# Kernel tuning notes

Measured on AMD Instinct MI355X. Metric: run time of the kernel, lower is better.

## Reference

```python
import jax, jax.numpy as jnp
from jax import lax
import numpy as np


def _lstm_stack(sequence, Wx, Wh, b):
    """Standard single-layer LSTM; returns all hidden states [B, T, H]."""
    B, T, I = sequence.shape
    H = Wh.shape[0]
    # Precompute input projection for all timesteps: [B, T, 4H]
    x_proj = jnp.einsum('bti,ih->bth', sequence, Wx) + b

    def step(carry, xt):  # xt: [B, 4H]
        h, c = carry
        z = xt + h @ Wh
        i, f, g, o = jnp.split(z, 4, axis=-1)
        i = jax.nn.sigmoid(i)
        f = jax.nn.sigmoid(f)
        g = jnp.tanh(g)
        o = jax.nn.sigmoid(o)
        c = f * c + i * g
        h = o * jnp.tanh(c)
        return (h, c), h

    h0 = jnp.zeros((B, H), dtype=sequence.dtype)
    c0 = jnp.zeros((B, H), dtype=sequence.dtype)
    (_, _), ys = lax.scan(step, (h0, c0), jnp.transpose(x_proj, (1, 0, 2)))
    return jnp.transpose(ys, (1, 0, 2))  # [B, T, H]


def setup_inputs() -> dict:
    key = jax.random.key(0)
    ks = jax.random.split(key, 6)
    B, T, I, H, K = 64, 256, 512, 1024, 512
    sequence = jax.random.normal(ks[0], (B, T, I), dtype=jnp.float32)
    n_iter = jax.random.randint(ks[1], (B,), 0, T, dtype=jnp.int32)
    Wx = jax.random.normal(ks[2], (I, 4 * H), dtype=jnp.float32) * 0.05
    Wh = jax.random.normal(ks[3], (H, 4 * H), dtype=jnp.float32) * 0.05
    b = jnp.zeros((4 * H,), dtype=jnp.float32)
    codebook = jax.random.normal(ks[4], (K, H), dtype=jnp.float32)
    return {"sequence": sequence, "n_iter": n_iter, "Wx": Wx, "Wh": Wh,
            "b": b, "codebook": codebook}


def reference(sequence, n_iter, Wx, Wh, b, codebook):
    B = sequence.shape[0]
    lstm_stack = _lstm_stack(sequence, Wx, Wh, b)          # [B, T, H]
    unquantized = lstm_stack[jnp.arange(B), n_iter]         # [B, H] batched gather
    # VQ: L2 distance to each codebook vector, argmin, embed lookup
    diff = unquantized[:, None, :] - codebook[None, :, :]   # [B, K, H]
    distance = jnp.linalg.norm(diff, axis=-1)               # [B, K]
    nearest_codebook_idxs = jnp.argmin(distance, axis=-1)   # [B]
    quantized = codebook[nearest_codebook_idxs]             # [B, H]
    return nearest_codebook_idxs, quantized, unquantized
```

## Files before the change

kernel.cpp:

```cpp
#include <hip/hip_runtime.h>
#include <hip/hip_cooperative_groups.h>

namespace cg = cooperative_groups;

typedef unsigned short u16;
typedef unsigned int   u32;
typedef unsigned long long u64;
typedef __attribute__((ext_vector_type(8))) short short8;
typedef __attribute__((ext_vector_type(4))) float f32x4;

#define BB   64
#define TT   256
#define II   512
#define HH   1024
#define KCB  512
#define GH   4096
#define KTOT 1536

#define BPAD 1544

#define WS_WT   0
#define WS_H    (GH*KTOT)
#define WS_DIST (WS_H + 131072)
#define WS_BARC (WS_DIST + BB*KCB)
#define WS_BART (WS_BARC + 8*9*32)

#define LD_AG(p)   __hip_atomic_load((p), __ATOMIC_RELAXED, __HIP_MEMORY_SCOPE_AGENT)
#define ST_AG(p,v) __hip_atomic_store((p), (v), __ATOMIC_RELAXED, __HIP_MEMORY_SCOPE_AGENT)

__device__ __forceinline__ float sigf(float x){ return 1.0f/(1.0f+expf(-x)); }
__device__ __forceinline__ u16 bf16r(float f){ u32 u = __float_as_uint(f); u += 0x7FFFu + ((u>>16)&1u); return (u16)(u>>16); }
__device__ __forceinline__ float bf16f(u16 h){ return __uint_as_float(((u32)h)<<16); }

__device__ __forceinline__ void bar_arrive(u32* bar, int bid, int tid, int e){
    asm volatile("s_waitcnt vmcnt(0)" ::: "memory");
    __syncthreads();
    if (tid == 0) {
        u32 old = atomicAdd(bar + (bid & 7) * 32, 1u);
        if (old == (u32)(e * 32 - 1)) {
            u32 old2 = atomicAdd(bar + 8 * 32, 1u);
            if (old2 == (u32)(e * 8 - 1)) {
                #pragma unroll
                for (int gg = 0; gg < 8; ++gg)
                    ST_AG(bar + (9 + gg) * 32, (u32)e);
            }
        }
    }
}
__device__ __forceinline__ void bar_wait(u32* bar, int bid, int tid, int e){
    if (tid == 0) {
        while ((int)LD_AG(bar + (9 + (bid & 7)) * 32) < e)
            __builtin_amdgcn_s_sleep(1);
        __builtin_amdgcn_fence(__ATOMIC_ACQUIRE, "agent");
    }
    __syncthreads();
}

__global__ __launch_bounds__(512, 1)
void lstm_vq(const float* __restrict__ seq, const int* __restrict__ nit,
             const float* __restrict__ Wx, const float* __restrict__ Wh,
             const float* __restrict__ bias, const float* __restrict__ cb,
             float* __restrict__ out, float* __restrict__ ws)
{
    cg::grid_group grid = cg::this_grid();
    __shared__ __align__(16) u16 bHi[16*BPAD];
    __shared__ __align__(16) u16 bLo[16*BPAD];
    __shared__ __align__(16) float exs[8*1024];
    __shared__ int permL[64], snitL[64];
    __shared__ int sBest;

    const int tid = threadIdx.x;
    const int l   = tid & 63;
    const int w   = tid >> 6;
    const int bid = (int)blockIdx.x;

    float* WT   = ws + WS_WT;
    u16*   hbuf = (u16*)(ws + WS_H);
    float* dist = ws + WS_DIST;
    u32*   barC = (u32*)(ws + WS_BARC);
    u32*   barT = (u32*)(ws + WS_BART);
    float* qz   = out + BB;
    float* uq   = out + BB + BB*HH;

    if (bid == 0) {
        for (int i = tid; i < 8*9*32 + 17*32; i += 512) ST_AG(barC + i, 0u);
    }

    {
        const int c0 = bid * 16;
        float* tile = (float*)bHi;
        for (int kt = 0; kt < KTOT; kt += 64) {
            __syncthreads();
            #pragma unroll
            for (int ii2 = 0; ii2 < 2; ++ii2) {
                int ky = ii2*32 + (tid>>4);
                int cx = tid & 15;
                int kk = kt + ky;
                float v = (kk < II) ? Wx[(size_t)kk*GH + c0 + cx]
                                    : Wh[(size_t)(kk-II)*GH + c0 + cx];
                tile[cx*68 + ky] = v;
            }
            __syncthreads();
            {
                int cx = tid >> 5;
                int k2 = (tid & 31) * 2;
                WT[(size_t)(c0+cx)*KTOT + kt + k2]     = tile[cx*68 + k2];
                WT[(size_t)(c0+cx)*KTOT + kt + k2 + 1] = tile[cx*68 + k2 + 1];
            }
        }
        grid.sync();
    }

    {
        __syncthreads();
        const int n  = tid >> 5;
        const int zc = ((n>>2)<<10) + (bid<<2) + (n&3);
        const float* wr = WT + (size_t)zc*KTOT;
        for (int k = (tid&31)*8; k < KTOT; k += 256) {
            f32x4 v0 = *(const f32x4*)(wr + k);
            f32x4 v1 = *(const f32x4*)(wr + k + 4);
            short8 ph, pl;
            #pragma unroll
            for (int e = 0; e < 8; ++e) {
                float fv = (e<4) ? v0[e] : v1[e-4];
                u16 hb = bf16r(fv);
                ph[e] = (short)hb;
                pl[e] = (short)bf16r(fv - bf16f(hb));
            }
            *(short8*)&bHi[n*BPAD + k] = ph;
            *(short8*)&bLo[n*BPAD + k] = pl;
        }
    }

    {
        if (w == 0) {
            int ni = nit[l];
            int r  = 0;
            #pragma unroll
            for (int j = 0; j < 64; ++j) {
                int nj = __shfl(ni, j, 64);
                r += (nj > ni || (nj == ni && j < l)) ? 1 : 0;
            }
            permL[r] = l;
            snitL[r] = ni;
        }
        __syncthreads();
    }

    const int rEx  = (tid & 255) >> 2;
    const int ccEx = tid & 3;
    const int hcol = (bid<<2) + ccEx;
    const int prG  = permL[rEx];
    const int myNs = snitL[rEx];

    const int tmx0 = __builtin_amdgcn_readfirstlane(snitL[0]);
    const int tmx1 = __builtin_amdgcn_readfirstlane(snitL[16]);
    const int tmx2 = __builtin_amdgcn_readfirstlane(snitL[32]);
    const int tmx3 = __builtin_amdgcn_readfirstlane(snitL[48]);
    const int maxN = tmx0;

    const int aPh0 = permL[ 0 + (l&15)];
    const int aPh1 = permL[16 + (l&15)];
    const int aPh2 = permL[32 + (l&15)];
    const int aPh3 = permL[48 + (l&15)];

    const float bi_ = bias[hcol], bf_ = bias[HH+hcol], bg_ = bias[2*HH+hcol], bo_ = bias[3*HH+hcol];

    const int ag   = (l>>4)<<3;
    const int bn   = l & 15;
    const int cprod = bid >> 5;
    u32* myArr  = barC + cprod*288;
    const u32* myFlag = barC + w*288 + (1 + (bid&7))*32;

    float cst = 0.0f;

#define XC(P, h0, h1, kab) { \
    short8 ph, pl; \
    _Pragma("unroll") for (int e=0;e<8;++e){ \
        float fv = (e<4) ? h0[e] : h1[e-4]; \
        u16 hb = bf16r(fv); ph[e]=(short)hb; pl[e]=(short)bf16r(fv - bf16f(hb)); } \
    int bo = bn*BPAD + (kab); \
    short8 bhv = *(const short8*)&bHi[bo]; \
    short8 blv = *(const short8*)&bLo[bo]; \
    P##0 = __builtin_amdgcn_mfma_f32_16x16x32_bf16(ph, bhv, P##0, 0,0,0); \
    P##1 = __builtin_amdgcn_mfma_f32_16x16x32_bf16(pl, bhv, P##1, 0,0,0); \
    P##2 = __builtin_amdgcn_mfma_f32_16x16x32_bf16(ph, blv, P##2, 0,0,0); }

#define HM(P, B, kab) { \
    int bo = bn*BPAD + (kab); \
    short8 bhv = *(const short8*)&bHi[bo]; \
    short8 blv = *(const short8*)&bLo[bo]; \
    P##0 = __builtin_amdgcn_mfma_f32_16x16x32_bf16(B##h, bhv, P##0, 0,0,0); \
    P##1 = __builtin_amdgcn_mfma_f32_16x16x32_bf16(B##l, bhv, P##1, 0,0,0); \
    P##2 = __builtin_amdgcn_mfma_f32_16x16x32_bf16(B##h, blv, P##2, 0,0,0); }

#define XPH(P, APH) { \
    const float* xp_ = seq + (size_t)(APH)*(TT*II) + (size_t)t*II + (w<<6) + ag; \
    f32x4 x0 = *(const f32x4*)xp_,      x1 = *(const f32x4*)(xp_+4); \
    f32x4 x2 = *(const f32x4*)(xp_+32), x3 = *(const f32x4*)(xp_+36); \
    XC(P, x0, x1, (w<<6)+ag); \
    XC(P, x2, x3, (w<<6)+32+ag); }

#define HPH(P, mt) { \
    const u16* hp_ = hiP + (size_t)(((mt)<<4)+(l&15))*HH + (w<<7) + ag; \
    short8 h0h = *(const short8*)hp_,       h0l = *(const short8*)(hp_+65536); \
    short8 h1h = *(const short8*)(hp_+32),  h1l = *(const short8*)(hp_+32+65536); \
    short8 h2h = *(const short8*)(hp_+64),  h2l = *(const short8*)(hp_+64+65536); \
    short8 h3h = *(const short8*)(hp_+96),  h3l = *(const short8*)(hp_+96+65536); \
    HM(P, h0, 512+(w<<7)+ag);    HM(P, h1, 512+(w<<7)+32+ag); \
    HM(P, h2, 512+(w<<7)+64+ag); HM(P, h3, 512+(w<<7)+96+ag); }

#define EXW(P, mt) { \
    const int n_ = l & 15; \
    const int r0_ = ((mt)<<4) + ((l>>4)<<2); \
    float* e_ = exs + w*1024 + r0_*16 + n_; \
    _Pragma("unroll") for (int j=0;j<4;++j) \
        e_[j*16] = P##0[j] + P##1[j] + P##2[j]; }

    for (int t = 0; t <= maxN; ++t) {
        const u16* hiP = hbuf + (size_t)(t&1)*131072;
        u16*       hiN = hbuf + (size_t)(1-(t&1))*131072;
        u16*       loN = hiN + 65536;

        f32x4 z4 = {0.f,0.f,0.f,0.f};
        f32x4 aA0=z4,aA1=z4,aA2=z4, aB0=z4,aB1=z4,aB2=z4;
        f32x4 aC0=z4,aC1=z4,aC2=z4, aD0=z4,aD1=z4,aD2=z4;

        XPH(aA, aPh0)
        if (t <= tmx1) { XPH(aB, aPh1) }
        if (t <= tmx2) { XPH(aC, aPh2) }
        if (t <= tmx3) { XPH(aD, aPh3) }

        if (t > 0) {
            while ((int)LD_AG(myFlag) < t) __builtin_amdgcn_s_sleep(1);
            HPH(aA,0)
            if (t <= tmx1) { HPH(aB,1) }
            if (t <= tmx2) { HPH(aC,2) }
            if (t <= tmx3) { HPH(aD,3) }
        }

        EXW(aA,0)
        if (t <= tmx1) { EXW(aB,1) }
        if (t <= tmx2) { EXW(aC,2) }
        if (t <= tmx3) { EXW(aD,3) }
        __syncthreads();

        if (tid < 256 && t <= myNs) {
            const float* e0 = exs + rEx*16 + ccEx;
            float z0 = bi_, z1 = bf_, z2 = bg_, z3 = bo_;
            #pragma unroll
            for (int ww = 0; ww < 8; ++ww) {
                const float* e_ = e0 + ww*1024;
                z0 += e_[0]; z1 += e_[4]; z2 += e_[8]; z3 += e_[12];
            }
            float iv = sigf(z0), fv = sigf(z1), gv = tanhf(z2), ov = sigf(z3);
            cst = fv*cst + iv*gv;
            float h = ov * tanhf(cst);
            u16 hb = bf16r(h);
            u16 lb = bf16r(h - bf16f(hb));
            ST_AG(&hiN[(size_t)rEx*HH + hcol], hb);
            ST_AG(&loN[(size_t)rEx*HH + hcol], lb);
            if (t == myNs) ST_AG(&uq[(size_t)prG*HH + hcol], h);
        }

        asm volatile("s_waitcnt vmcnt(0)" ::: "memory");
        __syncthreads();
        if (tid == 0) {
            u32 old = atomicAdd(myArr, 1u);
            if (old == (u32)((t+1)*32 - 1)) {
                #pragma unroll
                for (int g = 0; g < 8; ++g)
                    ST_AG(myArr + (1+g)*32, (u32)(t+1));
            }
            __builtin_amdgcn_fence(__ATOMIC_ACQUIRE, "agent");
        }
        __syncthreads();
    }

#undef XC
#undef HM
#undef XPH
#undef HPH
#undef EXW

    while ((int)LD_AG(myFlag) < maxN + 1) __builtin_amdgcn_s_sleep(1);
    __syncthreads();
    if (tid == 0) __builtin_amdgcn_fence(__ATOMIC_ACQUIRE, "agent");
    __syncthreads();

    {
        const int wid = bid*8 + w;
        for (int p = wid*16; p < wid*16 + 16; ++p) {
            int rr = p >> 9;
            int kk = p & 511;
            const u64* u8p = (const u64*)(uq + (size_t)rr*HH);
            const f32x4* c4 = (const f32x4*)(cb + (size_t)kk*HH);
            float s = 0.0f;
            #pragma unroll
            for (int q = 0; q < 4; ++q) {
                u64 e0 = u8p[2*(l + q*64)];
                u64 e1 = u8p[2*(l + q*64) + 1];
                f32x4 b = c4[l + q*64];
                float a0 = __uint_as_float((u32)e0), a1 = __uint_as_float((u32)(e0>>32));
                float a2 = __uint_as_float((u32)e1), a3 = __uint_as_float((u32)(e1>>32));
                float d0 = a0-b[0], d1 = a1-b[1], d2 = a2-b[2], d3 = a3-b[3];
                s += d0*d0 + d1*d1 + d2*d2 + d3*d3;
            }
            #pragma unroll
            for (int off = 32; off > 0; off >>= 1) s += __shfl_xor(s, off, 64);
            if (l == 0) ST_AG(&dist[(size_t)rr*KCB + kk], s);
        }
    }
    bar_arrive(barT, bid, tid, 1);
    bar_wait(barT, bid, tid, 1);

    if (bid < BB) {
        const int rr = bid;
        if (tid < 64) {
            float best = 3.4e38f;
            int   bi   = 0;
            for (int kk = tid; kk < KCB; kk += 64) {
                float v = dist[(size_t)rr*KCB + kk];
                if (v < best) { best = v; bi = kk; }
            }
            #pragma unroll
            for (int off = 32; off > 0; off >>= 1) {
                float ovv = __shfl_xor(best, off, 64);
                int   oii = __shfl_xor(bi,   off, 64);
                if (ovv < best || (ovv == best && oii < bi)) { best = ovv; bi = oii; }
            }
            if (tid == 0) { sBest = bi; out[rr] = (float)bi; }
        }
        __syncthreads();
        const int bk = sBest;
        const f32x4* c4 = (const f32x4*)(cb + (size_t)bk*HH);
        f32x4*       q4 = (f32x4*)(qz + (size_t)rr*HH);
        for (int d = tid; d < HH/4; d += 512) q4[d] = c4[d];
    }
}

extern "C" void kernel_launch(void* const* d_in, const int* in_sizes, int n_in,
                              void* d_out, int out_size, void* d_ws, size_t ws_size,
                              hipStream_t stream) {
    const float* seq  = (const float*)d_in[0];
    const int*   nit  = (const int*)  d_in[1];
    const float* Wx   = (const float*)d_in[2];
    const float* Wh   = (const float*)d_in[3];
    const float* bias = (const float*)d_in[4];
    const float* cb   = (const float*)d_in[5];
    float* out = (float*)d_out;
    float* ws  = (float*)d_ws;

    void* args[] = { &seq, &nit, &Wx, &Wh, &bias, &cb, &out, &ws };
    hipLaunchCooperativeKernel((void*)lstm_vq, dim3(256), dim3(512), args, 0, stream);
}
```

Baseline: 2.518 ms.

## Replace counter barrier with per-block flags, register-cache weights, double-buffer h loads

Each block now writes its own step flag, and each wave polls 32 flags in parallel with a wave-wide vote. This replaces the atomic counter plus broadcast barrier and removes the serialized atomic chain. The per-block B-operand weight fragments are loaded once into registers instead of re-read from LDS every step. The h loads are double-buffered so the next tile's global loads overlap the current MFMAs. The costs are higher register pressure and more global flag polling traffic.

New measurement: 2.534 ms. About the same (+0.6%).

```diff
diff --git a/kernel.cpp b/kernel.cpp
--- a/kernel.cpp
+++ b/kernel.cpp
@@ -22,8 +22,8 @@
 #define WS_WT   0
 #define WS_H    (GH*KTOT)
 #define WS_DIST (WS_H + 131072)
-#define WS_BARC (WS_DIST + BB*KCB)
-#define WS_BART (WS_BARC + 8*9*32)
+#define WS_FLG  (WS_DIST + BB*KCB)
+#define WS_BART (WS_FLG + 8*32)
 
 #define LD_AG(p)   __hip_atomic_load((p), __ATOMIC_RELAXED, __HIP_MEMORY_SCOPE_AGENT)
 #define ST_AG(p,v) __hip_atomic_store((p), (v), __ATOMIC_RELAXED, __HIP_MEMORY_SCOPE_AGENT)
@@ -77,13 +77,13 @@
     float* WT   = ws + WS_WT;
     u16*   hbuf = (u16*)(ws + WS_H);
     float* dist = ws + WS_DIST;
-    u32*   barC = (u32*)(ws + WS_BARC);
+    u32*   flg  = (u32*)(ws + WS_FLG);
     u32*   barT = (u32*)(ws + WS_BART);
     float* qz   = out + BB;
     float* uq   = out + BB + BB*HH;
 
     if (bid == 0) {
-        for (int i = tid; i < 8*9*32 + 17*32; i += 512) ST_AG(barC + i, 0u);
+        for (int i = tid; i < 8*32 + 17*32; i += 512) ST_AG(flg + i, 0u);
     }
 
     {
@@ -147,17 +147,33 @@
         __syncthreads();
     }
 
+    const int ag  = (l>>4)<<3;
+    const int bn  = l & 15;
+    const int xk0 = (w<<6) + ag;
+    const int hk0 = 512 + (w<<7) + ag;
+    const short8 bx0h = *(const short8*)&bHi[bn*BPAD + xk0];
+    const short8 bx0l = *(const short8*)&bLo[bn*BPAD + xk0];
+    const short8 bx1h = *(const short8*)&bHi[bn*BPAD + xk0 + 32];
+    const short8 bx1l = *(const short8*)&bLo[bn*BPAD + xk0 + 32];
+    const short8 bh0h = *(const short8*)&bHi[bn*BPAD + hk0];
+    const short8 bh0l = *(const short8*)&bLo[bn*BPAD + hk0];
+    const short8 bh1h = *(const short8*)&bHi[bn*BPAD + hk0 + 32];
+    const short8 bh1l = *(const short8*)&bLo[bn*BPAD + hk0 + 32];
+    const short8 bh2h = *(const short8*)&bHi[bn*BPAD + hk0 + 64];
+    const short8 bh2l = *(const short8*)&bLo[bn*BPAD + hk0 + 64];
+    const short8 bh3h = *(const short8*)&bHi[bn*BPAD + hk0 + 96];
+    const short8 bh3l = *(const short8*)&bLo[bn*BPAD + hk0 + 96];
+
     const int rEx  = (tid & 255) >> 2;
     const int ccEx = tid & 3;
     const int hcol = (bid<<2) + ccEx;
     const int prG  = permL[rEx];
     const int myNs = snitL[rEx];
 
-    const int tmx0 = __builtin_amdgcn_readfirstlane(snitL[0]);
     const int tmx1 = __builtin_amdgcn_readfirstlane(snitL[16]);
     const int tmx2 = __builtin_amdgcn_readfirstlane(snitL[32]);
     const int tmx3 = __builtin_amdgcn_readfirstlane(snitL[48]);
-    const int maxN = tmx0;
+    const int maxN = __builtin_amdgcn_readfirstlane(snitL[0]);
 
     const int aPh0 = permL[ 0 + (l&15)];
     const int aPh1 = permL[16 + (l&15)];
@@ -166,49 +182,50 @@
 
     const float bi_ = bias[hcol], bf_ = bias[HH+hcol], bg_ = bias[2*HH+hcol], bo_ = bias[3*HH+hcol];
 
-    const int ag   = (l>>4)<<3;
-    const int bn   = l & 15;
     const int cprod = bid >> 5;
-    u32* myArr  = barC + cprod*288;
-    const u32* myFlag = barC + w*288 + (1 + (bid&7))*32;
+    u32* myFlagW = flg + cprod*32 + (bid & 31);
+    const u32* pollP = flg + w*32 + (l & 31);
 
     float cst = 0.0f;
-
-#define XC(P, h0, h1, kab) { \
+    short8 hA0h,hA0l,hA1h,hA1l,hA2h,hA2l,hA3h,hA3l;
+    short8 hB0h,hB0l,hB1h,hB1l,hB2h,hB2l,hB3h,hB3l;
+
+#define XC2(P, v0, v1, BH, BL) { \
     short8 ph, pl; \
     _Pragma("unroll") for (int e=0;e<8;++e){ \
-        float fv = (e<4) ? h0[e] : h1[e-4]; \
+        float fv = (e<4) ? v0[e] : v1[e-4]; \
         u16 hb = bf16r(fv); ph[e]=(short)hb; pl[e]=(short)bf16r(fv - bf16f(hb)); } \
-    int bo = bn*BPAD + (kab); \
-    short8 bhv = *(const short8*)&bHi[bo]; \
-    short8 blv = *(const short8*)&bLo[bo]; \
-    P##0 = __builtin_amdgcn_mfma_f32_16x16x32_bf16(ph, bhv, P##0, 0,0,0); \
-    P##1 = __builtin_amdgcn_mfma_f32_16x16x32_bf16(pl, bhv, P##1, 0,0,0); \
-    P##2 = __builtin_amdgcn_mfma_f32_16x16x32_bf16(ph, blv, P##2, 0,0,0); }
-
-#define HM(P, B, kab) { \
-    int bo = bn*BPAD + (kab); \
-    short8 bhv = *(const short8*)&bHi[bo]; \
-    short8 blv = *(const short8*)&bLo[bo]; \
-    P##0 = __builtin_amdgcn_mfma_f32_16x16x32_bf16(B##h, bhv, P##0, 0,0,0); \
-    P##1 = __builtin_amdgcn_mfma_f32_16x16x32_bf16(B##l, bhv, P##1, 0,0,0); \
-    P##2 = __builtin_amdgcn_mfma_f32_16x16x32_bf16(B##h, blv, P##2, 0,0,0); }
+    P##0 = __builtin_amdgcn_mfma_f32_16x16x32_bf16(ph, BH, P##0, 0,0,0); \
+    P##1 = __builtin_amdgcn_mfma_f32_16x16x32_bf16(pl, BH, P##1, 0,0,0); \
+    P##2 = __builtin_amdgcn_mfma_f32_16x16x32_bf16(ph, BL, P##2, 0,0,0); }
 
 #define XPH(P, APH) { \
     const float* xp_ = seq + (size_t)(APH)*(TT*II) + (size_t)t*II + (w<<6) + ag; \
     f32x4 x0 = *(const f32x4*)xp_,      x1 = *(const f32x4*)(xp_+4); \
     f32x4 x2 = *(const f32x4*)(xp_+32), x3 = *(const f32x4*)(xp_+36); \
-    XC(P, x0, x1, (w<<6)+ag); \
-    XC(P, x2, x3, (w<<6)+32+ag); }
-
-#define HPH(P, mt) { \
+    XC2(P, x0, x1, bx0h, bx0l); \
+    XC2(P, x2, x3, bx1h, bx1l); }
+
+#define HLDP(BUF, mt) { \
     const u16* hp_ = hiP + (size_t)(((mt)<<4)+(l&15))*HH + (w<<7) + ag; \
-    short8 h0h = *(const short8*)hp_,       h0l = *(const short8*)(hp_+65536); \
-    short8 h1h = *(const short8*)(hp_+32),  h1l = *(const short8*)(hp_+32+65536); \
-    short8 h2h = *(const short8*)(hp_+64),  h2l = *(const short8*)(hp_+64+65536); \
-    short8 h3h = *(const short8*)(hp_+96),  h3l = *(const short8*)(hp_+96+65536); \
-    HM(P, h0, 512+(w<<7)+ag);    HM(P, h1, 512+(w<<7)+32+ag); \
-    HM(P, h2, 512+(w<<7)+64+ag); HM(P, h3, 512+(w<<7)+96+ag); }
+    BUF##0h = *(const short8*)hp_;       BUF##0l = *(const short8*)(hp_+65536); \
+    BUF##1h = *(const short8*)(hp_+32);  BUF##1l = *(const short8*)(hp_+32+65536); \
+    BUF##2h = *(const short8*)(hp_+64);  BUF##2l = *(const short8*)(hp_+64+65536); \
+    BUF##3h = *(const short8*)(hp_+96);  BUF##3l = *(const short8*)(hp_+96+65536); }
+
+#define HMMP(BUF, P) { \
+    P##0 = __builtin_amdgcn_mfma_f32_16x16x32_bf16(BUF##0h, bh0h, P##0, 0,0,0); \
+    P##1 = __builtin_amdgcn_mfma_f32_16x16x32_bf16(BUF##0l, bh0h, P##1, 0,0,0); \
+    P##2 = __builtin_amdgcn_mfma_f32_16x16x32_bf16(BUF##0h, bh0l, P##2, 0,0,0); \
+    P##0 = __builtin_amdgcn_mfma_f32_16x16x32_bf16(BUF##1h, bh1h, P##0, 0,0,0); \
+    P##1 = __builtin_amdgcn_mfma_f32_16x16x32_bf16(BUF##1l, bh1h, P##1, 0,0,0); \
+    P##2 = __builtin_amdgcn_mfma_f32_16x16x32_bf16(BUF##1h, bh1l, P##2, 0,0,0); \
+    P##0 = __builtin_amdgcn_mfma_f32_16x16x32_bf16(BUF##2h, bh2h, P##0, 0,0,0); \
+    P##1 = __builtin_amdgcn_mfma_f32_16x16x32_bf16(BUF##2l, bh2h, P##1, 0,0,0); \
+    P##2 = __builtin_amdgcn_mfma_f32_16x16x32_bf16(BUF##2h, bh2l, P##2, 0,0,0); \
+    P##0 = __builtin_amdgcn_mfma_f32_16x16x32_bf16(BUF##3h, bh3h, P##0, 0,0,0); \
+    P##1 = __builtin_amdgcn_mfma_f32_16x16x32_bf16(BUF##3l, bh3h, P##1, 0,0,0); \
+    P##2 = __builtin_amdgcn_mfma_f32_16x16x32_bf16(BUF##3h, bh3l, P##2, 0,0,0); }
 
 #define EXW(P, mt) { \
     const int n_ = l & 15; \
@@ -232,11 +249,23 @@
         if (t <= tmx3) { XPH(aD, aPh3) }
 
         if (t > 0) {
-            while ((int)LD_AG(myFlag) < t) __builtin_amdgcn_s_sleep(1);
-            HPH(aA,0)
-            if (t <= tmx1) { HPH(aB,1) }
-            if (t <= tmx2) { HPH(aC,2) }
-            if (t <= tmx3) { HPH(aD,3) }
+            for (;;) {
+                u32 v = LD_AG(pollP);
+                if (__all((int)v >= t)) break;
+                __builtin_amdgcn_s_sleep(1);
+            }
+            HLDP(hA, 0)
+            if (t <= tmx1) { HLDP(hB, 1) }
+            HMMP(hA, aA)
+            if (t <= tmx1) {
+                if (t <= tmx2) { HLDP(hA, 2) }
+                HMMP(hB, aB)
+                if (t <= tmx2) {
+                    if (t <= tmx3) { HLDP(hB, 3) }
+                    HMMP(hA, aC)
+                    if (t <= tmx3) { HMMP(hB, aD) }
+                }
+            }
         }
 
         EXW(aA,0)
@@ -266,27 +295,20 @@
         asm volatile("s_waitcnt vmcnt(0)" ::: "memory");
         __syncthreads();
         if (tid == 0) {
-            u32 old = atomicAdd(myArr, 1u);
-            if (old == (u32)((t+1)*32 - 1)) {
-                #pragma unroll
-                for (int g = 0; g < 8; ++g)
-                    ST_AG(myArr + (1+g)*32, (u32)(t+1));
-            }
+            ST_AG(myFlagW, (u32)(t + 1));
             __builtin_amdgcn_fence(__ATOMIC_ACQUIRE, "agent");
         }
         __syncthreads();
     }
 
-#undef XC
-#undef HM
+#undef XC2
 #undef XPH
-#undef HPH
+#undef HLDP
+#undef HMMP
 #undef EXW
 
-    while ((int)LD_AG(myFlag) < maxN + 1) __builtin_amdgcn_s_sleep(1);
-    __syncthreads();
-    if (tid == 0) __builtin_amdgcn_fence(__ATOMIC_ACQUIRE, "agent");
-    __syncthreads();
+    bar_arrive(barT, bid, tid, 1);
+    bar_wait(barT, bid, tid, 1);
 
     {
         const int wid = bid*8 + w;
@@ -311,8 +333,8 @@
             if (l == 0) ST_AG(&dist[(size_t)rr*KCB + kk], s);
         }
     }
-    bar_arrive(barT, bid, tid, 1);
-    bar_wait(barT, bid, tid, 1);
+    bar_arrive(barT, bid, tid, 2);
+    bar_wait(barT, bid, tid, 2);
 
     if (bid < BB) {
         const int rr = bid;
```
